# Kernel tuning notes

Hardware: AMD Instinct MI355X
Metric: run time of the kernel (lower is better)

The kernel has to match this reference:

```python
import jax, jax.numpy as jnp
import numpy as np

T, N, D = 8, 2048, 64
H, NH = 128, 4        # hidden_dim, num_heads (flax default num_heads=4)
HD = H // NH
TE = 16               # time_embedding_dim
OUT = 64              # final output_dim
E = D + TE            # enhanced node feature dim


def _params(key):
    ks = jax.random.split(key, 16)
    s = 0.05
    w = lambda k, shape: jax.random.normal(k, shape, jnp.float32) * s
    return dict(
        time_freq=w(ks[0], (T, TE // 2)) * 2.0,
        Wq=w(ks[1], (T, E, H)), bq=jnp.zeros((T, H), jnp.float32),
        Wk=w(ks[2], (T, E, H)), bk=jnp.zeros((T, H), jnp.float32),
        Wv=w(ks[3], (T, E, H)), bv=jnp.zeros((T, H), jnp.float32),
        ln_g=jnp.ones((T, H), jnp.float32), ln_b=jnp.zeros((T, H), jnp.float32),
        W1=w(ks[4], (T, H, 2 * H)), b1=jnp.zeros((T, 2 * H), jnp.float32),
        W2=w(ks[5], (T, 2 * H, H)), b2=jnp.zeros((T, H), jnp.float32),
        Wr=w(ks[6], (T, 2 * H, H)), br=jnp.zeros((T, H), jnp.float32),
        Wz=w(ks[7], (T, 2 * H, H)), bz=jnp.zeros((T, H), jnp.float32),
        Wn=w(ks[8], (T, 2 * H, H)), bn=jnp.zeros((T, H), jnp.float32),
        Wout=w(ks[9], (H, OUT)), bout=jnp.zeros((OUT,), jnp.float32),
    )


def setup_inputs() -> dict:
    key = jax.random.key(0)
    k0, k1, k2, k3, kp = jax.random.split(key, 5)
    inp = dict(
        node_sequence=jax.random.normal(k0, (T, N, D), jnp.float32),
        adjacency_sequence=(jax.random.uniform(k1, (T, N, N)) < 0.02).astype(jnp.float32),
        timestamps=jax.random.uniform(k2, (T, N), jnp.float32) * 100.0,
        edge_sequence=jax.random.randint(k3, (T, 32768, 2), 0, N),  # unused in math
    )
    inp.update(_params(kp))
    return inp


def _forward(node_sequence, adjacency_sequence, timestamps, time_freq,
             Wq, bq, Wk, bk, Wv, bv, ln_g, ln_b, W1, b1, W2, b2,
             Wr, br, Wz, bz, Wn, bn, Wout, bout):
    eye = jnp.eye(N, dtype=jnp.float32)
    inv_sqrt_hd = np.float32(1.0 / np.sqrt(HD))

    def step(h, xs):
        (nodes, adj, ts, tf, wq, bq_, wk, bk_, wv, bv_, g, b,
         w1, b1_, w2, b2_, wr, br_, wz, bz_, wn, bn_) = xs
        # sinusoidal time encoding -> enhanced node features [N, D+TE]
        ang = ts[:, None] * tf[None, :]
        enh = jnp.concatenate([nodes, jnp.sin(ang), jnp.cos(ang)], axis=-1)
        # the original builds per-head Dense projections in a Python loop;
        # concatenating them equals one [E,H] projection split into heads
        q = (enh @ wq + bq_).reshape(N, NH, HD)
        k = (enh @ wk + bk_).reshape(N, NH, HD)
        v = (enh @ wv + bv_).reshape(N, NH, HD)
        scores = jnp.einsum('nhd,mhd->hnm', q, k) * inv_sqrt_hd  # [NH,N,N]
        decay = jnp.exp(-jnp.abs(ts[:, None] - ts[None, :]) / 10.0)
        scores = scores * decay[None]
        mask = (adj + eye) > 0
        scores = jnp.where(mask[None], scores, -jnp.inf)
        attn = jax.nn.softmax(scores, axis=-1)
        mh = jnp.einsum('hnm,mhd->nhd', attn, v).reshape(N, H)
        # residual skipped: mh dim (128) != enhanced dim (80), as in source
        mu = mh.mean(-1, keepdims=True)
        var = mh.var(-1, keepdims=True)
        mh = (mh - mu) * jax.lax.rsqrt(var + 1e-6) * g + b  # LayerNorm eps=1e-6
        ff = jax.nn.gelu(mh @ w1 + b1_) @ w2 + b2_  # inner output_dim == hidden_dim
        # GRU cell
        hx = jnp.concatenate([h, ff], axis=-1)
        r = jax.nn.sigmoid(hx @ wr + br_)
        z = jax.nn.sigmoid(hx @ wz + bz_)
        n_ = jnp.tanh(jnp.concatenate([r * h, ff], axis=-1) @ wn + bn_)
        return (1.0 - z) * n_ + z * h, None

    xs = (node_sequence, adjacency_sequence, timestamps, time_freq,
          Wq, bq, Wk, bk, Wv, bv, ln_g, ln_b, W1, b1, W2, b2,
          Wr, br, Wz, bz, Wn, bn)
    h0 = jnp.zeros((N, H), jnp.float32)
    h, _ = jax.lax.scan(step, h0, xs)
    return h @ Wout + bout  # [N, OUT]


def reference(node_sequence, adjacency_sequence, timestamps, edge_sequence,
              time_freq, Wq, bq, Wk, bk, Wv, bv, ln_g, ln_b,
              W1, b1, W2, b2, Wr, br, Wz, bz, Wn, bn, Wout, bout):
    # edge_sequence is accepted by the original forward but never used
    return _forward(node_sequence, adjacency_sequence, timestamps, time_freq,
                    Wq, bq, Wk, bk, Wv, bv, ln_g, ln_b, W1, b1, W2, b2,
                    Wr, br, Wz, bz, Wn, bn, Wout, bout)
```

## Files before the change

kernel.cpp:

```cpp
#include <hip/hip_runtime.h>
#include <math.h>

#define T 8
#define N 2048
#define D 64
#define H 128
#define NH 4
#define HD 32
#define TE 16
#define OUT 64
#define E 80
#define NBCAP 128

typedef float f4v __attribute__((ext_vector_type(4)));
typedef __attribute__((ext_vector_type(8))) short bf16x8;
typedef __attribute__((ext_vector_type(4))) float f32x4;

__device__ __forceinline__ float gelu_tanh(float x){
    float x3 = x*x*x;
    float t = tanhf(0.7978845608028654f*(x + 0.044715f*x3));
    return 0.5f*x*(1.0f+t);
}
__device__ __forceinline__ float sigmoidf_(float x){ return 1.0f/(1.0f+expf(-x)); }
__device__ __forceinline__ unsigned short f2bf(float x){
    unsigned u = __float_as_uint(x);
    return (unsigned short)((u + 0x7FFFu + ((u>>16)&1u)) >> 16);
}

__global__ __launch_bounds__(256) void k_compact(
    const float* __restrict__ adj, unsigned short* __restrict__ nb, int* __restrict__ cnt)
{
    int wid  = threadIdx.x >> 6;
    int lane = threadIdx.x & 63;
    int row  = blockIdx.x*4 + wid;
    int n = row & 2047;
    const f4v* arow4 = (const f4v*)(adj + (size_t)row*(size_t)N);

    f4v a4[8];
    #pragma unroll
    for (int it=0; it<8; it++) a4[it] = __builtin_nontemporal_load(arow4 + it*64 + lane);

    unsigned short* nbr = nb + (size_t)row*NBCAP;
    int c = 0;
    unsigned long long lt = (1ull<<lane)-1ull;
    #pragma unroll
    for (int it = 0; it < 8; it++){
        int m0 = it*256 + lane*4;
        bool f0 = (a4[it].x>0.f) || (m0   == n);
        bool f1 = (a4[it].y>0.f) || (m0+1 == n);
        bool f2 = (a4[it].z>0.f) || (m0+2 == n);
        bool f3 = (a4[it].w>0.f) || (m0+3 == n);
        unsigned long long b0=__ballot(f0), b1=__ballot(f1), b2=__ballot(f2), b3=__ballot(f3);
        int before = __popcll(b0&lt)+__popcll(b1&lt)+__popcll(b2&lt)+__popcll(b3&lt);
        int pos = c + before;
        if (f0 && pos<NBCAP) nbr[pos] = (unsigned short)(m0  );  pos += f0;
        if (f1 && pos<NBCAP) nbr[pos] = (unsigned short)(m0+1);  pos += f1;
        if (f2 && pos<NBCAP) nbr[pos] = (unsigned short)(m0+2);  pos += f2;
        if (f3 && pos<NBCAP) nbr[pos] = (unsigned short)(m0+3);  pos += f3;
        c += __popcll(b0)+__popcll(b1)+__popcll(b2)+__popcll(b3);
    }
    if (lane == 0) cnt[row] = (c > NBCAP) ? NBCAP : c;
}

__global__ __launch_bounds__(64) void k_wswz(
    const float* __restrict__ W1, const float* __restrict__ W2,
    const float* __restrict__ Wr, const float* __restrict__ Wz, const float* __restrict__ Wn,
    unsigned short* __restrict__ W1s, unsigned short* __restrict__ W2s,
    unsigned short* __restrict__ Wrs, unsigned short* __restrict__ Wzs, unsigned short* __restrict__ Wns,
    unsigned short* __restrict__ Wrt, unsigned short* __restrict__ Wzt, unsigned short* __restrict__ Wnt)
{
    int b = blockIdx.x;
    const float* src; unsigned short* dst; int NT,KB,ncol,koff;
    if (b < 512)      {          src=W1; dst=W1s; NT=16; KB=4; ncol=256; koff=0;   }
    else if (b < 1024){ b-=512;  src=W2; dst=W2s; NT=8;  KB=8; ncol=128; koff=0;   }
    else if (b < 1280){ b-=1024; src=Wr; dst=Wrs; NT=8;  KB=4; ncol=128; koff=128; }
    else if (b < 1536){ b-=1280; src=Wz; dst=Wzs; NT=8;  KB=4; ncol=128; koff=128; }
    else if (b < 1792){ b-=1536; src=Wn; dst=Wns; NT=8;  KB=4; ncol=128; koff=128; }
    else if (b < 2048){ b-=1792; src=Wr; dst=Wrt; NT=8;  KB=4; ncol=128; koff=0;   }
    else if (b < 2304){ b-=2048; src=Wz; dst=Wzt; NT=8;  KB=4; ncol=128; koff=0;   }
    else              { b-=2304; src=Wn; dst=Wnt; NT=8;  KB=4; ncol=128; koff=0;   }
    int fpt = NT*KB;
    int t = b / fpt, rem = b % fpt, nt = rem / KB, kb = rem % KB;
    int lane = threadIdx.x;
    int kk = koff + kb*32 + (lane>>4)*8;
    int n  = nt*16 + (lane&15);
    const float* s = src + (size_t)t*32768;
    bf16x8 o;
    #pragma unroll
    for (int j=0;j<8;j++) o[j] = (short)f2bf(s[(size_t)(kk+j)*ncol + n]);
    *(bf16x8*)(dst + ((size_t)b*64 + lane)*8) = o;
}

__global__ __launch_bounds__(256) void k_qkv(
    const float* __restrict__ nodes, const float* __restrict__ ts, const float* __restrict__ tf,
    const float* __restrict__ Wq, const float* __restrict__ bq,
    const float* __restrict__ Wk, const float* __restrict__ bk,
    const float* __restrict__ Wv, const float* __restrict__ bv,
    float* __restrict__ q, float* __restrict__ k, float* __restrict__ v)
{
    const int BR = 16;
    __shared__ float A[BR*E];
    int t  = blockIdx.x >> 7;
    int n0 = (blockIdx.x & 127) * BR;
    int tid = threadIdx.x;
    for (int idx = tid; idx < BR*E; idx += 256){
        int r = idx / E, e = idx - r*E;
        int n = n0 + r;
        float val;
        if (e < D) val = nodes[((size_t)(t*N+n))*D + e];
        else {
            int j = (e - D) & 7;
            float ang = ts[t*N+n] * tf[t*(TE/2)+j];
            val = (e < D+8) ? sinf(ang) : cosf(ang);
        }
        A[idx] = val;
    }
    __syncthreads();
    for (int jj = tid; jj < 3*H; jj += 256){
        int sel = jj >> 7, j = jj & 127;
        const float* W = (sel==0?Wq:(sel==1?Wk:Wv)) + (size_t)t*E*H;
        const float* B = (sel==0?bq:(sel==1?bk:bv)) + t*H;
        float acc[BR];
        float bias = B[j];
        #pragma unroll
        for (int r=0;r<BR;r++) acc[r]=bias;
        for (int e=0;e<E;e+=4){
            float w0=W[(e+0)*H+j], w1=W[(e+1)*H+j], w2=W[(e+2)*H+j], w3=W[(e+3)*H+j];
            #pragma unroll
            for (int r=0;r<BR;r++){
                float4 a = *(const float4*)&A[r*E+e];
                acc[r] += a.x*w0 + a.y*w1 + a.z*w2 + a.w*w3;
            }
        }
        float* outp = (sel==0?q:(sel==1?k:v));
        #pragma unroll
        for (int r=0;r<BR;r++) outp[((size_t)(t*N+n0+r))*H + j] = acc[r];
    }
}

__global__ __launch_bounds__(256) void k_attn(
    const unsigned short* __restrict__ nb, const int* __restrict__ cntp,
    const float* __restrict__ ts,
    const float* __restrict__ q, const float* __restrict__ k, const float* __restrict__ v,
    const float* __restrict__ ln_g, const float* __restrict__ ln_b,
    float* __restrict__ mhn)
{
    __shared__ unsigned short nb_s[4][NBCAP];
    __shared__ float sc_s[4][64][NH];
    __shared__ float qrow_s[4][H];

    int wid  = threadIdx.x >> 6;
    int lane = threadIdx.x & 63;
    int t = blockIdx.x & 7;
    int n = (blockIdx.x >> 3)*4 + wid;
    int row = t*N + n;
    size_t rowbase = (size_t)row;
    float tsn = ts[row];
    int cnt = cntp[row];

    for (int i = lane; i < cnt; i += 64) nb_s[wid][i] = nb[rowbase*NBCAP + i];
    qrow_s[wid][lane]    = q[rowbase*H + lane];
    qrow_s[wid][lane+64] = q[rowbase*H + lane + 64];
    __builtin_amdgcn_wave_barrier();

    const float inv_sqrt_hd = 0.17677669529663687f;
    const float NEG = -3.402823466e38f;
    int g   = lane >> 4;
    int l16 = lane & 15;
    int hd  = l16 >> 2;
    int hh16 = lane >> 4;

    f4v q0 = *(const f4v*)&qrow_s[wid][l16*8];
    f4v q1 = *(const f4v*)&qrow_s[wid][l16*8+4];

    float mR0=NEG,mR1=NEG,mR2=NEG,mR3=NEG;
    float sR0=0.f,sR1=0.f,sR2=0.f,sR3=0.f;
    f4v accA = {0.f,0.f,0.f,0.f}, accB = {0.f,0.f,0.f,0.f};

    for (int cb = 0; cb < cnt; cb += 64){
        int cc = min(64, cnt - cb);
        for (int i0 = 0; i0 < cc; i0 += 4){
            int jn = i0 + g;
            bool act = jn < cc;
            float part = 0.f;
            int m = 0;
            if (act){
                m = nb_s[wid][cb + jn];
                const f4v* kp = (const f4v*)(k + ((size_t)t*N + m)*H + l16*8);
                f4v k0 = kp[0], k1 = kp[1];
                part = q0.x*k0.x + q0.y*k0.y + q0.z*k0.z + q0.w*k0.w
                     + q1.x*k1.x + q1.y*k1.y + q1.z*k1.z + q1.w*k1.w;
            }
            part += __shfl_xor(part, 1);
            part += __shfl_xor(part, 2);
            if (act && (l16 & 3) == 0){
                float dt = fabsf(tsn - ts[t*N + m]);
                float w  = expf(-dt*0.1f) * inv_sqrt_hd;
                sc_s[wid][jn][l16>>2] = part * w;
            }
        }
        __builtin_amdgcn_wave_barrier();
        float mx = NEG;
        for (int i = l16; i < cc; i += 16) mx = fmaxf(mx, sc_s[wid][i][hh16]);
        #pragma unroll
        for (int off=8; off; off>>=1) mx = fmaxf(mx, __shfl_xor(mx, off, 16));
        float h0m=__shfl(mx,0), h1m=__shfl(mx,16), h2m=__shfl(mx,32), h3m=__shfl(mx,48);
        float n0=fmaxf(mR0,h0m), n1=fmaxf(mR1,h1m), n2=fmaxf(mR2,h2m), n3=fmaxf(mR3,h3m);
        float e0=expf(mR0-n0), e1=expf(mR1-n1), e2=expf(mR2-n2), e3=expf(mR3-n3);
        float nh = (hh16==0)?n0:((hh16==1)?n1:((hh16==2)?n2:n3));
        float sum = 0.f;
        for (int i = l16; i < cc; i += 16){
            float p = expf(sc_s[wid][i][hh16] - nh);
            sc_s[wid][i][hh16] = p;
            sum += p;
        }
        #pragma unroll
        for (int off=8; off; off>>=1) sum += __shfl_xor(sum, off, 16);
        float su0=__shfl(sum,0), su1=__shfl(sum,16), su2=__shfl(sum,32), su3=__shfl(sum,48);
        sR0 = sR0*e0 + su0; sR1 = sR1*e1 + su1;
        sR2 = sR2*e2 + su2; sR3 = sR3*e3 + su3;
        mR0=n0; mR1=n1; mR2=n2; mR3=n3;
        float eh = (hd==0)?e0:((hd==1)?e1:((hd==2)?e2:e3));
        accA *= eh; accB *= eh;
        __builtin_amdgcn_wave_barrier();
        for (int i0 = 0; i0 < cc; i0 += 4){
            int jn = i0 + g;
            if (jn < cc){
                int m = nb_s[wid][cb + jn];
                const f4v* vp = (const f4v*)(v + ((size_t)t*N + m)*H + l16*8);
                f4v v0 = vp[0], v1 = vp[1];
                float p = sc_s[wid][jn][hd];
                accA += p * v0;
                accB += p * v1;
            }
        }
        __builtin_amdgcn_wave_barrier();
    }

    #pragma unroll
    for (int off = 16; off <= 32; off <<= 1){
        accA.x += __shfl_xor(accA.x, off); accA.y += __shfl_xor(accA.y, off);
        accA.z += __shfl_xor(accA.z, off); accA.w += __shfl_xor(accA.w, off);
        accB.x += __shfl_xor(accB.x, off); accB.y += __shfl_xor(accB.y, off);
        accB.z += __shfl_xor(accB.z, off); accB.w += __shfl_xor(accB.w, off);
    }
    float sh = (hd==0)?sR0:((hd==1)?sR1:((hd==2)?sR2:sR3));
    float inv = 1.f / sh;
    accA *= inv; accB *= inv;

    float ls = accA.x+accA.y+accA.z+accA.w + accB.x+accB.y+accB.z+accB.w;
    #pragma unroll
    for (int off=8; off; off>>=1) ls += __shfl_xor(ls, off, 16);
    float mu = ls * (1.f/128.f);
    f4v dA = accA - mu, dB = accB - mu;
    float vs = dA.x*dA.x+dA.y*dA.y+dA.z*dA.z+dA.w*dA.w
             + dB.x*dB.x+dB.y*dB.y+dB.z*dB.z+dB.w*dB.w;
    #pragma unroll
    for (int off=8; off; off>>=1) vs += __shfl_xor(vs, off, 16);
    float rs = rsqrtf(vs*(1.f/128.f) + 1e-6f);

    if (g == 0){
        const f4v* gp = (const f4v*)(ln_g + t*H + l16*8);
        const f4v* bp = (const f4v*)(ln_b + t*H + l16*8);
        f4v g0 = gp[0], g1 = gp[1], b0 = bp[0], b1 = bp[1];
        f4v o0 = dA*rs*g0 + b0;
        f4v o1 = dB*rs*g1 + b1;
        f4v* op = (f4v*)(mhn + rowbase*H + l16*8);
        op[0] = o0; op[1] = o1;
    }
}

#define ULD 264
__global__ __launch_bounds__(256) void k_ffpre(
    const float* __restrict__ mhn,
    const unsigned short* __restrict__ W1s, const float* __restrict__ b1,
    const unsigned short* __restrict__ W2s, const float* __restrict__ b2,
    const unsigned short* __restrict__ Wrs, const float* __restrict__ br,
    const unsigned short* __restrict__ Wzs, const float* __restrict__ bz,
    const unsigned short* __restrict__ Wns, const float* __restrict__ bn,
    float* __restrict__ fr, float* __restrict__ fz, float* __restrict__ fn)
{
    __shared__ unsigned short U_lds[32*ULD];
    int tid = threadIdx.x;
    int w = tid >> 6, lane = tid & 63;
    int t = blockIdx.x & 7;
    int n0 = (blockIdx.x >> 3) * 32;
    int li = lane & 15, ls = lane >> 4;

    bf16x8 af[2][4];
    const float* Abase = mhn + (size_t)(t*N + n0)*H;
    #pragma unroll
    for (int mt=0; mt<2; mt++){
        #pragma unroll
        for (int kb=0; kb<4; kb++){
            const float* p = Abase + (size_t)(mt*16 + li)*H + kb*32 + ls*8;
            float4 x0 = *(const float4*)p;
            float4 x1 = *(const float4*)(p+4);
            bf16x8 a;
            a[0]=(short)f2bf(x0.x); a[1]=(short)f2bf(x0.y); a[2]=(short)f2bf(x0.z); a[3]=(short)f2bf(x0.w);
            a[4]=(short)f2bf(x1.x); a[5]=(short)f2bf(x1.y); a[6]=(short)f2bf(x1.z); a[7]=(short)f2bf(x1.w);
            af[mt][kb] = a;
        }
    }

    const bf16x8* W1f = (const bf16x8*)W1s;
    #pragma unroll
    for (int u=0; u<4; u++){
        int nt = w*4 + u;
        f32x4 c0 = {0.f,0.f,0.f,0.f}, c1 = {0.f,0.f,0.f,0.f};
        #pragma unroll
        for (int kb=0; kb<4; kb++){
            bf16x8 b = W1f[((t*16 + nt)*4 + kb)*64 + lane];
            c0 = __builtin_amdgcn_mfma_f32_16x16x32_bf16(af[0][kb], b, c0, 0,0,0);
            c1 = __builtin_amdgcn_mfma_f32_16x16x32_bf16(af[1][kb], b, c1, 0,0,0);
        }
        float bias = b1[t*256 + nt*16 + li];
        #pragma unroll
        for (int i=0;i<4;i++){
            U_lds[(     ls*4+i)*ULD + nt*16 + li] = f2bf(gelu_tanh(c0[i] + bias));
            U_lds[(16 + ls*4+i)*ULD + nt*16 + li] = f2bf(gelu_tanh(c1[i] + bias));
        }
    }
    __syncthreads();

    const bf16x8* W2f = (const bf16x8*)W2s;
    f32x4 c2[2][2];
    #pragma unroll
    for (int u=0;u<2;u++){ c2[u][0] = (f32x4){0.f,0.f,0.f,0.f}; c2[u][1] = (f32x4){0.f,0.f,0.f,0.f}; }
    for (int kb=0; kb<8; kb++){
        bf16x8 a0 = *(const bf16x8*)&U_lds[(     li)*ULD + kb*32 + ls*8];
        bf16x8 a1 = *(const bf16x8*)&U_lds[(16 + li)*ULD + kb*32 + ls*8];
        #pragma unroll
        for (int u=0; u<2; u++){
            int nt = w*2 + u;
            bf16x8 b = W2f[((t*8 + nt)*8 + kb)*64 + lane];
            c2[u][0] = __builtin_amdgcn_mfma_f32_16x16x32_bf16(a0, b, c2[u][0], 0,0,0);
            c2[u][1] = __builtin_amdgcn_mfma_f32_16x16x32_bf16(a1, b, c2[u][1], 0,0,0);
        }
    }
    __syncthreads();
    #pragma unroll
    for (int u=0; u<2; u++){
        int nt = w*2 + u;
        float bias = b2[t*128 + nt*16 + li];
        #pragma unroll
        for (int i=0;i<4;i++){
            U_lds[(     ls*4+i)*ULD + nt*16 + li] = f2bf(c2[u][0][i] + bias);
            U_lds[(16 + ls*4+i)*ULD + nt*16 + li] = f2bf(c2[u][1][i] + bias);
        }
    }
    __syncthreads();

    bf16x8 aF[2][4];
    #pragma unroll
    for (int mt=0; mt<2; mt++)
        #pragma unroll
        for (int kb=0; kb<4; kb++)
            aF[mt][kb] = *(const bf16x8*)&U_lds[(mt*16 + li)*ULD + kb*32 + ls*8];

    #pragma unroll
    for (int u=0; u<6; u++){
        int unit = w*6 + u;
        int gate = unit >> 3, nt = unit & 7;
        const bf16x8* Wf = (const bf16x8*)(gate==0 ? Wrs : (gate==1 ? Wzs : Wns));
        const float*  Bv = gate==0 ? br : (gate==1 ? bz : bn);
        float* outp      = gate==0 ? fr : (gate==1 ? fz : fn);
        f32x4 c0 = {0.f,0.f,0.f,0.f}, c1 = {0.f,0.f,0.f,0.f};
        #pragma unroll
        for (int kb=0; kb<4; kb++){
            bf16x8 b = Wf[((t*8 + nt)*4 + kb)*64 + lane];
            c0 = __builtin_amdgcn_mfma_f32_16x16x32_bf16(aF[0][kb], b, c0, 0,0,0);
            c1 = __builtin_amdgcn_mfma_f32_16x16x32_bf16(aF[1][kb], b, c1, 0,0,0);
        }
        float bias = Bv[t*128 + nt*16 + li];
        #pragma unroll
        for (int i=0;i<4;i++){
            outp[(size_t)(t*N + n0 +      ls*4+i)*H + nt*16 + li] = c0[i] + bias;
            outp[(size_t)(t*N + n0 + 16 + ls*4+i)*H + nt*16 + li] = c1[i] + bias;
        }
    }
}

#define HLD 132
__global__ __launch_bounds__(256) void k_gru_mfma(
    const float* __restrict__ fr, const float* __restrict__ fz, const float* __restrict__ fn,
    const unsigned short* __restrict__ Wrt, const unsigned short* __restrict__ Wzt,
    const unsigned short* __restrict__ Wnt,
    const float* __restrict__ Wout, const float* __restrict__ bout,
    float* __restrict__ out)
{
    __shared__ float Hs[16*HLD], Rl[16*HLD], Zl[16*HLD], RH[16*HLD];
    int tid = threadIdx.x;
    int w = tid >> 6, lane = tid & 63;
    int li = lane & 15, ls = lane >> 4;
    int n0 = blockIdx.x * 16;
    for (int idx = tid; idx < 16*HLD; idx += 256) Hs[idx] = 0.f;
    __syncthreads();

    for (int t = 0; t < T; t++){
        bf16x8 af[4];
        #pragma unroll
        for (int kb=0; kb<4; kb++){
            const float* p = &Hs[li*HLD + kb*32 + ls*8];
            float4 x0 = *(const float4*)p, x1 = *(const float4*)(p+4);
            bf16x8 a;
            a[0]=(short)f2bf(x0.x); a[1]=(short)f2bf(x0.y); a[2]=(short)f2bf(x0.z); a[3]=(short)f2bf(x0.w);
            a[4]=(short)f2bf(x1.x); a[5]=(short)f2bf(x1.y); a[6]=(short)f2bf(x1.z); a[7]=(short)f2bf(x1.w);
            af[kb] = a;
        }
        #pragma unroll
        for (int u=0; u<4; u++){
            int unit = w*4 + u;
            int gate = unit >> 3, nt = unit & 7;
            const bf16x8* Wf = (const bf16x8*)(gate ? Wzt : Wrt);
            const float*  P  = gate ? fz : fr;
            f32x4 c;
            #pragma unroll
            for (int i=0;i<4;i++) c[i] = P[(size_t)(t*N + n0 + ls*4+i)*H + nt*16 + li];
            #pragma unroll
            for (int kb=0; kb<4; kb++){
                bf16x8 b = Wf[((t*8 + nt)*4 + kb)*64 + lane];
                c = __builtin_amdgcn_mfma_f32_16x16x32_bf16(af[kb], b, c, 0,0,0);
            }
            float* Dst = gate ? Zl : Rl;
            #pragma unroll
            for (int i=0;i<4;i++) Dst[(ls*4+i)*HLD + nt*16 + li] = sigmoidf_(c[i]);
        }
        __syncthreads();
        for (int idx = tid; idx < 16*128; idx += 256){
            int r = idx >> 7, cc = idx & 127;
            RH[r*HLD + cc] = Rl[r*HLD + cc] * Hs[r*HLD + cc];
        }
        __syncthreads();
        bf16x8 an[4];
        #pragma unroll
        for (int kb=0; kb<4; kb++){
            const float* p = &RH[li*HLD + kb*32 + ls*8];
            float4 x0 = *(const float4*)p, x1 = *(const float4*)(p+4);
            bf16x8 a;
            a[0]=(short)f2bf(x0.x); a[1]=(short)f2bf(x0.y); a[2]=(short)f2bf(x0.z); a[3]=(short)f2bf(x0.w);
            a[4]=(short)f2bf(x1.x); a[5]=(short)f2bf(x1.y); a[6]=(short)f2bf(x1.z); a[7]=(short)f2bf(x1.w);
            an[kb] = a;
        }
        #pragma unroll
        for (int u=0; u<2; u++){
            int nt = w*2 + u;
            f32x4 c;
            #pragma unroll
            for (int i=0;i<4;i++) c[i] = fn[(size_t)(t*N + n0 + ls*4+i)*H + nt*16 + li];
            #pragma unroll
            for (int kb=0; kb<4; kb++){
                bf16x8 b = Wnt[0] , *dummy = 0;
                (void)dummy;
                bf16x8 bb = ((const bf16x8*)Wnt)[((t*8 + nt)*4 + kb)*64 + lane];
                c = __builtin_amdgcn_mfma_f32_16x16x32_bf16(an[kb], bb, c, 0,0,0);
            }
            #pragma unroll
            for (int i=0;i<4;i++){
                int ridx = (ls*4+i)*HLD + nt*16 + li;
                float nv = tanhf(c[i]);
                float zz = Zl[ridx];
                Hs[ridx] = (1.f - zz)*nv + zz*Hs[ridx];
            }
        }
        __syncthreads();
    }

    {
        int j = tid & 63, rq = tid >> 6;
        #pragma unroll
        for (int rr=0; rr<4; rr++){
            int r = rq*4 + rr;
            float acc = bout[j];
            for (int e=0; e<H; e+=4){
                float4 a = *(const float4*)&Hs[r*HLD + e];
                acc += a.x*Wout[(e+0)*OUT+j] + a.y*Wout[(e+1)*OUT+j]
                     + a.z*Wout[(e+2)*OUT+j] + a.w*Wout[(e+3)*OUT+j];
            }
            out[(size_t)(n0 + r)*OUT + j] = acc;
        }
    }
}

extern "C" void kernel_launch(void* const* d_in, const int* in_sizes, int n_in,
                              void* d_out, int out_size, void* d_ws, size_t ws_size,
                              hipStream_t stream)
{
    const float* nodes = (const float*)d_in[0];
    const float* adj   = (const float*)d_in[1];
    const float* ts    = (const float*)d_in[2];
    const float* tf    = (const float*)d_in[4];
    const float* Wq = (const float*)d_in[5];  const float* bq = (const float*)d_in[6];
    const float* Wk = (const float*)d_in[7];  const float* bk = (const float*)d_in[8];
    const float* Wv = (const float*)d_in[9];  const float* bv = (const float*)d_in[10];
    const float* lng = (const float*)d_in[11]; const float* lnb = (const float*)d_in[12];
    const float* W1 = (const float*)d_in[13]; const float* b1 = (const float*)d_in[14];
    const float* W2 = (const float*)d_in[15]; const float* b2 = (const float*)d_in[16];
    const float* Wr = (const float*)d_in[17]; const float* br = (const float*)d_in[18];
    const float* Wz = (const float*)d_in[19]; const float* bz = (const float*)d_in[20];
    const float* Wn = (const float*)d_in[21]; const float* bn = (const float*)d_in[22];
    const float* Wout = (const float*)d_in[23]; const float* bout = (const float*)d_in[24];
    float* out = (float*)d_out;

    const size_t TNH = (size_t)T*N*H;
    float* ws  = (float*)d_ws;
    float* q   = ws;
    float* k   = q  + TNH;
    float* v   = k  + TNH;
    float* mhn = v  + TNH;
    float* fr  = mhn+ TNH;
    float* fz  = fr + TNH;
    float* fn  = fz + TNH;
    unsigned short* nb = (unsigned short*)(fn + TNH);
    int* cnt = (int*)(nb + (size_t)T*N*NBCAP);
    unsigned short* W1s = (unsigned short*)(cnt + T*N);
    unsigned short* W2s = W1s + 262144;
    unsigned short* Wrs = W2s + 262144;
    unsigned short* Wzs = Wrs + 131072;
    unsigned short* Wns = Wzs + 131072;
    unsigned short* Wrt = Wns + 131072;
    unsigned short* Wzt = Wrt + 131072;
    unsigned short* Wnt = Wzt + 131072;

    k_wswz<<<dim3(2560), dim3(64), 0, stream>>>(W1,W2,Wr,Wz,Wn, W1s,W2s,Wrs,Wzs,Wns, Wrt,Wzt,Wnt);
    k_compact<<<dim3(T*N/4), dim3(256), 0, stream>>>(adj, nb, cnt);
    k_qkv<<<dim3(T*(N/16)), dim3(256), 0, stream>>>(nodes, ts, tf, Wq,bq, Wk,bk, Wv,bv, q,k,v);
    k_attn<<<dim3(T*N/4), dim3(256), 0, stream>>>(nb, cnt, ts, q,k,v, lng,lnb, mhn);
    k_ffpre<<<dim3(512), dim3(256), 0, stream>>>(mhn, W1s,b1, W2s,b2, Wrs,br, Wzs,bz, Wns,bn, fr,fz,fn);
    k_gru_mfma<<<dim3(N/16), dim3(256), 0, stream>>>(fr,fz,fn, Wrt,Wzt,Wnt, Wout,bout, out);
}
```

Before: 167.6 us.

## Store GRU pre-activations in bf16, prefetch next step, fuse r*h into gate epilogue

The precomputed GRU input projections (fr, fz, fn) are now written in bf16 instead of fp32, halving the intermediate traffic between the feed-forward kernel and the recurrent kernel. The GRU kernel register-prefetches the next timestep's projections double-buffered across the unrolled time loop, hiding global latency on the serial recurrence. It also computes r*h directly in the sigmoid epilogue, removing the Rl buffer, one elementwise pass and one barrier per step. The bf16 storage adds rounding to the pre-activations, and the prefetch arrays raise register pressure.

```diff
diff --git a/kernel.cpp b/kernel.cpp
--- a/kernel.cpp
+++ b/kernel.cpp
@@ -25,6 +25,9 @@
 __device__ __forceinline__ unsigned short f2bf(float x){
     unsigned u = __float_as_uint(x);
     return (unsigned short)((u + 0x7FFFu + ((u>>16)&1u)) >> 16);
+}
+__device__ __forceinline__ float bf2f(unsigned short x){
+    return __uint_as_float(((unsigned)x) << 16);
 }
 
 __global__ __launch_bounds__(256) void k_compact(
@@ -278,7 +281,7 @@
     const unsigned short* __restrict__ Wrs, const float* __restrict__ br,
     const unsigned short* __restrict__ Wzs, const float* __restrict__ bz,
     const unsigned short* __restrict__ Wns, const float* __restrict__ bn,
-    float* __restrict__ fr, float* __restrict__ fz, float* __restrict__ fn)
+    unsigned short* __restrict__ fr, unsigned short* __restrict__ fz, unsigned short* __restrict__ fn)
 {
     __shared__ unsigned short U_lds[32*ULD];
     int tid = threadIdx.x;
@@ -364,7 +367,7 @@
         int gate = unit >> 3, nt = unit & 7;
         const bf16x8* Wf = (const bf16x8*)(gate==0 ? Wrs : (gate==1 ? Wzs : Wns));
         const float*  Bv = gate==0 ? br : (gate==1 ? bz : bn);
-        float* outp      = gate==0 ? fr : (gate==1 ? fz : fn);
+        unsigned short* outp = gate==0 ? fr : (gate==1 ? fz : fn);
         f32x4 c0 = {0.f,0.f,0.f,0.f}, c1 = {0.f,0.f,0.f,0.f};
         #pragma unroll
         for (int kb=0; kb<4; kb++){
@@ -375,29 +378,69 @@
         float bias = Bv[t*128 + nt*16 + li];
         #pragma unroll
         for (int i=0;i<4;i++){
-            outp[(size_t)(t*N + n0 +      ls*4+i)*H + nt*16 + li] = c0[i] + bias;
-            outp[(size_t)(t*N + n0 + 16 + ls*4+i)*H + nt*16 + li] = c1[i] + bias;
+            outp[(size_t)(t*N + n0 +      ls*4+i)*H + nt*16 + li] = f2bf(c0[i] + bias);
+            outp[(size_t)(t*N + n0 + 16 + ls*4+i)*H + nt*16 + li] = f2bf(c1[i] + bias);
         }
     }
 }
 
 #define HLD 132
 __global__ __launch_bounds__(256) void k_gru_mfma(
-    const float* __restrict__ fr, const float* __restrict__ fz, const float* __restrict__ fn,
+    const unsigned short* __restrict__ fr, const unsigned short* __restrict__ fz,
+    const unsigned short* __restrict__ fn,
     const unsigned short* __restrict__ Wrt, const unsigned short* __restrict__ Wzt,
     const unsigned short* __restrict__ Wnt,
     const float* __restrict__ Wout, const float* __restrict__ bout,
     float* __restrict__ out)
 {
-    __shared__ float Hs[16*HLD], Rl[16*HLD], Zl[16*HLD], RH[16*HLD];
+    __shared__ float Hs[16*HLD], Zl[16*HLD], RH[16*HLD];
     int tid = threadIdx.x;
     int w = tid >> 6, lane = tid & 63;
     int li = lane & 15, ls = lane >> 4;
     int n0 = blockIdx.x * 16;
+    int gateA = w >> 1;
     for (int idx = tid; idx < 16*HLD; idx += 256) Hs[idx] = 0.f;
     __syncthreads();
 
+    unsigned short pA[2][4][4];
+    unsigned short pC[2][2][4];
+
+    #pragma unroll
+    for (int u=0; u<4; u++){
+        int unit = w*4 + u, nt = unit & 7;
+        const unsigned short* P = (unit>>3) ? fz : fr;
+        #pragma unroll
+        for (int i=0;i<4;i++)
+            pA[0][u][i] = P[(size_t)(n0 + ls*4+i)*H + nt*16 + li];
+    }
+    #pragma unroll
+    for (int u=0; u<2; u++){
+        int nt = w*2 + u;
+        #pragma unroll
+        for (int i=0;i<4;i++)
+            pC[0][u][i] = fn[(size_t)(n0 + ls*4+i)*H + nt*16 + li];
+    }
+
+    #pragma unroll
     for (int t = 0; t < T; t++){
+        const int cur = t & 1, nxt = cur ^ 1;
+        if (t+1 < T){
+            #pragma unroll
+            for (int u=0; u<4; u++){
+                int unit = w*4 + u, nt = unit & 7;
+                const unsigned short* P = (unit>>3) ? fz : fr;
+                #pragma unroll
+                for (int i=0;i<4;i++)
+                    pA[nxt][u][i] = P[(size_t)((t+1)*N + n0 + ls*4+i)*H + nt*16 + li];
+            }
+            #pragma unroll
+            for (int u=0; u<2; u++){
+                int nt = w*2 + u;
+                #pragma unroll
+                for (int i=0;i<4;i++)
+                    pC[nxt][u][i] = fn[(size_t)((t+1)*N + n0 + ls*4+i)*H + nt*16 + li];
+            }
+        }
         bf16x8 af[4];
         #pragma unroll
         for (int kb=0; kb<4; kb++){
@@ -408,28 +451,25 @@
             a[4]=(short)f2bf(x1.x); a[5]=(short)f2bf(x1.y); a[6]=(short)f2bf(x1.z); a[7]=(short)f2bf(x1.w);
             af[kb] = a;
         }
+        const bf16x8* WfA = (const bf16x8*)(gateA ? Wzt : Wrt);
         #pragma unroll
         for (int u=0; u<4; u++){
-            int unit = w*4 + u;
-            int gate = unit >> 3, nt = unit & 7;
-            const bf16x8* Wf = (const bf16x8*)(gate ? Wzt : Wrt);
-            const float*  P  = gate ? fz : fr;
+            int nt = (w*4 + u) & 7;
             f32x4 c;
             #pragma unroll
-            for (int i=0;i<4;i++) c[i] = P[(size_t)(t*N + n0 + ls*4+i)*H + nt*16 + li];
+            for (int i=0;i<4;i++) c[i] = bf2f(pA[cur][u][i]);
             #pragma unroll
             for (int kb=0; kb<4; kb++){
-                bf16x8 b = Wf[((t*8 + nt)*4 + kb)*64 + lane];
+                bf16x8 b = WfA[((t*8 + nt)*4 + kb)*64 + lane];
                 c = __builtin_amdgcn_mfma_f32_16x16x32_bf16(af[kb], b, c, 0,0,0);
             }
-            float* Dst = gate ? Zl : Rl;
-            #pragma unroll
-            for (int i=0;i<4;i++) Dst[(ls*4+i)*HLD + nt*16 + li] = sigmoidf_(c[i]);
-        }
-        __syncthreads();
-        for (int idx = tid; idx < 16*128; idx += 256){
-            int r = idx >> 7, cc = idx & 127;
-            RH[r*HLD + cc] = Rl[r*HLD + cc] * Hs[r*HLD + cc];
+            #pragma unroll
+            for (int i=0;i<4;i++){
+                int idx = (ls*4+i)*HLD + nt*16 + li;
+                float s = sigmoidf_(c[i]);
+                if (gateA) Zl[idx] = s;
+                else       RH[idx] = s * Hs[idx];
+            }
         }
         __syncthreads();
         bf16x8 an[4];
@@ -447,13 +487,11 @@
             int nt = w*2 + u;
             f32x4 c;
             #pragma unroll
-            for (int i=0;i<4;i++) c[i] = fn[(size_t)(t*N + n0 + ls*4+i)*H + nt*16 + li];
+            for (int i=0;i<4;i++) c[i] = bf2f(pC[cur][u][i]);
             #pragma unroll
             for (int kb=0; kb<4; kb++){
-                bf16x8 b = Wnt[0] , *dummy = 0;
-                (void)dummy;
-                bf16x8 bb = ((const bf16x8*)Wnt)[((t*8 + nt)*4 + kb)*64 + lane];
-                c = __builtin_amdgcn_mfma_f32_16x16x32_bf16(an[kb], bb, c, 0,0,0);
+                bf16x8 b = ((const bf16x8*)Wnt)[((t*8 + nt)*4 + kb)*64 + lane];
+                c = __builtin_amdgcn_mfma_f32_16x16x32_bf16(an[kb], b, c, 0,0,0);
             }
             #pragma unroll
             for (int i=0;i<4;i++){
@@ -508,10 +546,10 @@
     float* k   = q  + TNH;
     float* v   = k  + TNH;
     float* mhn = v  + TNH;
-    float* fr  = mhn+ TNH;
-    float* fz  = fr + TNH;
-    float* fn  = fz + TNH;
-    unsigned short* nb = (unsigned short*)(fn + TNH);
+    unsigned short* frh = (unsigned short*)(mhn + TNH);
+    unsigned short* fzh = frh + TNH;
+    unsigned short* fnh = fzh + TNH;
+    unsigned short* nb  = fnh + TNH;
     int* cnt = (int*)(nb + (size_t)T*N*NBCAP);
     unsigned short* W1s = (unsigned short*)(cnt + T*N);
     unsigned short* W2s = W1s + 262144;
@@ -526,6 +564,6 @@
     k_compact<<<dim3(T*N/4), dim3(256), 0, stream>>>(adj, nb, cnt);
     k_qkv<<<dim3(T*(N/16)), dim3(256), 0, stream>>>(nodes, ts, tf, Wq,bq, Wk,bk, Wv,bv, q,k,v);
     k_attn<<<dim3(T*N/4), dim3(256), 0, stream>>>(nb, cnt, ts, q,k,v, lng,lnb, mhn);
-    k_ffpre<<<dim3(512), dim3(256), 0, stream>>>(mhn, W1s,b1, W2s,b2, Wrs,br, Wzs,bz, Wns,bn, fr,fz,fn);
-    k_gru_mfma<<<dim3(N/16), dim3(256), 0, stream>>>(fr,fz,fn, Wrt,Wzt,Wnt, Wout,bout, out);
-}
+    k_ffpre<<<dim3(512), dim3(256), 0, stream>>>(mhn, W1s,b1, W2s,b2, Wrs,br, Wzs,bz, Wns,bn, frh,fzh,fnh);
+    k_gru_mfma<<<dim3(N/16), dim3(256), 0, stream>>>(frh,fzh,fnh, Wrt,Wzt,Wnt, Wout,bout, out);
+}
```

Result: slower. 180.0 us (+7.3%).
